# Optimization experiments

Measured on AMD Instinct MI355X. Metric: run time of the kernel, lower is better.

The kernel has to match this reference:

```python
import jax, jax.numpy as jnp
import numpy as np

IN_DIM = 128
OUT_DIM = 128
BATCH = 1024
K = 3        # spline order
INIT_G = 3   # initial number of grid intervals


def setup_inputs() -> dict:
    key = jax.random.key(0)
    k1, k2 = jax.random.split(key)
    x = jax.random.normal(k1, (BATCH, IN_DIM), dtype=jnp.float32)
    # grid as in __init__: arange(-k, G+k+1)*h + (-1), tiled per (in,out) edge
    h = (1.0 - (-1.0)) / INIT_G
    grid_row = jnp.arange(-K, INIT_G + K + 1, dtype=jnp.float32) * h - 1.0  # (G+2k+1,) = (10,)
    grid = jnp.tile(grid_row[None, :], (IN_DIM * OUT_DIM, 1))               # (E, 10)
    n_basis = grid.shape[1] - 1 - K                                          # 6
    c_basis = 0.1 * jax.random.normal(k2, (IN_DIM * OUT_DIM, n_basis), dtype=jnp.float32)
    c_spl = jnp.ones(IN_DIM * OUT_DIM, dtype=jnp.float32)
    c_res = jnp.ones(IN_DIM * OUT_DIM, dtype=jnp.float32)
    return {"x": x, "grid": grid, "c_basis": c_basis, "c_spl": c_spl, "c_res": c_res}


def get_spline_basis(x_ext, grid, k=K):
    # x_ext: (E, B), grid: (E, G)
    g = grid[:, :, None]      # (E, G, 1)
    x = x_ext[:, None, :]     # (E, 1, B)
    b = ((x >= g[:, :-1]) & (x < g[:, 1:])).astype(x_ext.dtype)  # (E, G-1, B)
    for KK in range(1, k + 1):  # Cox-de Boor recursion; k is a small static constant
        left = (x - g[:, :-(KK + 1)]) / (g[:, KK:-1] - g[:, :-(KK + 1)])
        right = (g[:, KK + 1:] - x) / (g[:, KK + 1:] - g[:, 1:-KK])
        b = left * b[:, :-1] + right * b[:, 1:]
    return b  # (E, G-1-k, B)


def reference(x, grid, c_basis, c_spl, c_res):
    batch, in_dim = x.shape
    out_dim = c_spl.shape[0] // in_dim
    # broadcast each input feature to every output: edge index = o*in_dim + i
    x_ext = jnp.broadcast_to(x[:, None, :], (batch, out_dim, in_dim)).reshape(batch, in_dim * out_dim).T  # (E, B)
    res = jax.nn.swish(x_ext).T                                  # (B, E) residual activation
    Bi = get_spline_basis(x_ext, grid, K)                        # (E, 6, B)
    spl = jnp.einsum('ej,ejb->eb', c_basis, Bi).T                # (B, E)
    y = c_spl[None, :] * spl + c_res[None, :] * res              # (B, E)
    y = y.reshape(batch, out_dim, in_dim).sum(axis=2) / in_dim   # (B, out_dim)
    grid_r = grid.reshape(out_dim, in_dim, -1)
    input_norm = grid_r[:, :, -1] - grid_r[:, :, 0] + 1e-05      # (out, in)
    spl_reg = jnp.mean(jnp.abs(spl.reshape(batch, out_dim, in_dim)), axis=0) / input_norm
    return (y, spl_reg)
```

## Files before the change

kernel.cpp:

```cpp
#include <hip/hip_runtime.h>

static constexpr int BATCH   = 1024;
static constexpr int IN_DIM  = 128;
static constexpr int OUT_DIM = 128;
static constexpr int NEDGE   = IN_DIM * OUT_DIM;
static constexpr int Y_SIZE  = BATCH * OUT_DIM;

static constexpr size_t F_OFF  = 0;
static constexpr size_t WY_OFF = (size_t)128 * 1024 * 8;
static constexpr size_t WR_OFF = WY_OFF + (size_t)NEDGE * 8;
static constexpr size_t P_OFF  = WR_OFF + (size_t)NEDGE * 8;
static constexpr size_t C_OFF  = P_OFF + (size_t)NEDGE * 4;
static constexpr size_t P2_OFF = C_OFF + 128;

__global__ __launch_bounds__(256) void k_features(
    const float* __restrict__ x, const float* __restrict__ grid,
    const float* __restrict__ c_basis, const float* __restrict__ c_spl,
    const float* __restrict__ c_res, float* __restrict__ ws)
{
    __shared__ float xs[4][129];
    const int t  = threadIdx.x;
    const int b0 = blockIdx.x * 4;

#pragma unroll
    for (int k = 0; k < 2; ++k) {
        const int f = k * 256 + t;
        xs[f >> 7][f & 127] = x[(size_t)(b0 + (f >> 7)) * IN_DIM + (f & 127)];
    }

    float tg[10];
#pragma unroll
    for (int m = 0; m < 10; ++m) tg[m] = grid[m];

    float inv1[9], inv2[8], inv3[7];
#pragma unroll
    for (int m = 0; m < 9; ++m) inv1[m] = 1.0f / (tg[m + 1] - tg[m]);
#pragma unroll
    for (int m = 0; m < 8; ++m) inv2[m] = 1.0f / (tg[m + 2] - tg[m]);
#pragma unroll
    for (int m = 0; m < 7; ++m) inv3[m] = 1.0f / (tg[m + 3] - tg[m]);

    __syncthreads();

    float4* F4 = reinterpret_cast<float4*>(ws + F_OFF);
    const int brel  = t & 3;
    const int ibase = t >> 2;

#pragma unroll
    for (int k = 0; k < 2; ++k) {
        const int   i  = ibase + k * 64;
        const float xv = xs[brel][i];

        float bb[9];
#pragma unroll
        for (int m = 0; m < 9; ++m)
            bb[m] = (xv >= tg[m] && xv < tg[m + 1]) ? 1.0f : 0.0f;
#pragma unroll
        for (int m = 0; m < 8; ++m)
            bb[m] = (xv - tg[m]) * inv1[m] * bb[m]
                  + (tg[m + 2] - xv) * inv1[m + 1] * bb[m + 1];
#pragma unroll
        for (int m = 0; m < 7; ++m)
            bb[m] = (xv - tg[m]) * inv2[m] * bb[m]
                  + (tg[m + 3] - xv) * inv2[m + 1] * bb[m + 1];
#pragma unroll
        for (int m = 0; m < 6; ++m)
            bb[m] = (xv - tg[m]) * inv3[m] * bb[m]
                  + (tg[m + 4] - xv) * inv3[m + 1] * bb[m + 1];

        const float sw = xv / (1.0f + expf(-xv));
        const size_t g = (size_t)i * 1024 + b0 + brel;
        F4[g * 2 + 0] = make_float4(bb[0], bb[1], bb[2], bb[3]);
        F4[g * 2 + 1] = make_float4(bb[4], bb[5], sw, 0.0f);
    }

    if (t < 64) {
        const int e = blockIdx.x * 64 + t;
        float cb[6];
#pragma unroll
        for (int j = 0; j < 6; ++j) cb[j] = c_basis[(size_t)e * 6 + j];
        const float cs = c_spl[e];
        const float cr = c_res[e];
        const float invfac = 1.0f / ((float)BATCH * (tg[9] - tg[0] + 1e-5f));
        float4* Wy4 = reinterpret_cast<float4*>(ws + WY_OFF);
        float4* Wr4 = reinterpret_cast<float4*>(ws + WR_OFF);
        Wy4[(size_t)e * 2 + 0] = make_float4(cs * cb[0], cs * cb[1], cs * cb[2], cs * cb[3]);
        Wy4[(size_t)e * 2 + 1] = make_float4(cs * cb[4], cs * cb[5], cr, 0.0f);
        Wr4[(size_t)e * 2 + 0] = make_float4(cb[0], cb[1], cb[2], cb[3]);
        Wr4[(size_t)e * 2 + 1] = make_float4(cb[4], cb[5], invfac, 0.0f);
    }
}

__global__ __launch_bounds__(256) void k_main(
    const float* __restrict__ ws_c, float* __restrict__ ws_m)
{
    __shared__ float4 smem4[4096];
    const int t   = threadIdx.x;
    const int blk = blockIdx.x;
    const float4* F4 = reinterpret_cast<const float4*>(ws_c + F_OFF);

    if (blk < 256) {
        const float4* Wy4 = reinterpret_cast<const float4*>(ws_c + WY_OFF);
        const int bt = blk >> 4;
        const int ot = (blk >> 3) & 1;
        const int ic = blk & 7;
        const int b0 = bt * 64, o0 = ot * 64, i0 = ic * 16;
        float4* Fl = smem4;
        float4* Wl = smem4 + 2048;

#pragma unroll
        for (int r = 0; r < 8; ++r) {
            const int idx = r * 256 + t;
            const int ii = idx >> 7, w = idx & 127;
            Fl[ii * 128 + (w ^ ((w >> 3) & 1))] =
                F4[(size_t)(i0 + ii) * 2048 + b0 * 2 + w];
        }
#pragma unroll
        for (int r = 0; r < 8; ++r) {
            const int idx = r * 256 + t;
            const int oo = idx >> 5, w = idx & 31;
            Wl[oo * 32 + (w ^ (((oo >> 2) & 3) << 1))] =
                Wy4[(size_t)(o0 + oo) * 256 + i0 * 2 + w];
        }
        __syncthreads();

        const int bi = t & 15;
        const int og = t >> 4;
        float acc[4][4];
#pragma unroll
        for (int c = 0; c < 4; ++c)
#pragma unroll
            for (int q = 0; q < 4; ++q) acc[c][q] = 0.f;

#pragma unroll 2
        for (int ii = 0; ii < 16; ++ii) {
            float4 fb[4][2], wo[4][2];
#pragma unroll
            for (int c = 0; c < 4; ++c) {
                const int b  = bi + 16 * c;
                const int xr = (b >> 2) & 1;
                fb[c][0] = Fl[ii * 128 + ((b * 2)     ^ xr)];
                fb[c][1] = Fl[ii * 128 + ((b * 2 + 1) ^ xr)];
            }
#pragma unroll
            for (int q = 0; q < 4; ++q) {
                const int o  = og * 4 + q;
                const int xr = (og & 3) << 1;
                wo[q][0] = Wl[o * 32 + ((ii * 2)     ^ xr)];
                wo[q][1] = Wl[o * 32 + ((ii * 2 + 1) ^ xr)];
            }
#pragma unroll
            for (int c = 0; c < 4; ++c)
#pragma unroll
                for (int q = 0; q < 4; ++q) {
                    acc[c][q] += fb[c][0].x * wo[q][0].x + fb[c][0].y * wo[q][0].y
                               + fb[c][0].z * wo[q][0].z + fb[c][0].w * wo[q][0].w
                               + fb[c][1].x * wo[q][1].x + fb[c][1].y * wo[q][1].y
                               + fb[c][1].z * wo[q][1].z + fb[c][1].w * wo[q][1].w;
                }
        }

        float4* P2 = reinterpret_cast<float4*>(ws_m + P2_OFF);
#pragma unroll
        for (int c = 0; c < 4; ++c)
            P2[((size_t)ic * Y_SIZE
                + (size_t)(b0 + bi + 16 * c) * OUT_DIM + o0 + og * 4) >> 2] =
                make_float4(acc[c][0], acc[c][1], acc[c][2], acc[c][3]);
    } else {
        float4* Flds    = smem4;
        float*  partial = reinterpret_cast<float*>(smem4 + 512);
        const int rb = blk - 256;
        const int i  = rb >> 2;
        const int bq = rb & 3;
        const float4* src = F4 + ((size_t)i * 1024 + bq * 256) * 2;
        Flds[t]       = src[t];
        Flds[t + 256] = src[t + 256];

        const int o  = t & 127;
        const int bh = t >> 7;
        const int e  = (o << 7) + i;
        const float4* Wr4 = reinterpret_cast<const float4*>(ws_c + WR_OFF);
        const float4 w0 = Wr4[(size_t)e * 2 + 0];
        const float4 w1 = Wr4[(size_t)e * 2 + 1];
        __syncthreads();

        const float4* fl = &Flds[bh * 256];
        float acc = 0.f;
#pragma unroll 4
        for (int bl = 0; bl < 128; ++bl) {
            const float4 f0 = fl[bl * 2 + 0];
            const float4 f1 = fl[bl * 2 + 1];
            const float spl = f0.x * w0.x + f0.y * w0.y + f0.z * w0.z + f0.w * w0.w
                            + f1.x * w1.x + f1.y * w1.y;
            acc += fabsf(spl);
        }
        partial[t] = acc;
        __syncthreads();
        if (t < 128)
            ws_m[P_OFF + ((size_t)e << 2) + bq] = partial[t] + partial[t + 128];
    }
}

__global__ __launch_bounds__(256) void k_final(
    const float* __restrict__ ws, const float* __restrict__ grid,
    float* __restrict__ out)
{
    const int t   = threadIdx.x;
    const int blk = blockIdx.x;
    if (blk < 128) {
        const int gid = blk * 256 + t;
        const float4* P2 = reinterpret_cast<const float4*>(ws + P2_OFF);
        float4 s = P2[gid];
#pragma unroll
        for (int ic = 1; ic < 8; ++ic) {
            const float4 p = P2[(size_t)ic * (Y_SIZE / 4) + gid];
            s.x += p.x; s.y += p.y; s.z += p.z; s.w += p.w;
        }
        const float sc = 1.0f / (float)IN_DIM;
        reinterpret_cast<float4*>(out)[gid] =
            make_float4(s.x * sc, s.y * sc, s.z * sc, s.w * sc);
    } else {
        const int e = (blk - 128) * 256 + t;
        const float4 p = reinterpret_cast<const float4*>(ws + P_OFF)[e];
        const float invfac = 1.0f / ((float)BATCH * (grid[9] - grid[0] + 1e-5f));
        out[Y_SIZE + e] = (p.x + p.y + p.z + p.w) * invfac;
    }
}

extern "C" void kernel_launch(void* const* d_in, const int* in_sizes, int n_in,
                              void* d_out, int out_size, void* d_ws, size_t ws_size,
                              hipStream_t stream)
{
    const float* x  = (const float*)d_in[0];
    const float* gr = (const float*)d_in[1];
    const float* cb = (const float*)d_in[2];
    const float* cs = (const float*)d_in[3];
    const float* cr = (const float*)d_in[4];
    float* out = (float*)d_out;
    float* ws  = (float*)d_ws;

    k_features<<<256, 256, 0, stream>>>(x, gr, cb, cs, cr, ws);
    k_main<<<768, 256, 0, stream>>>(ws, ws);
    k_final<<<192, 256, 0, stream>>>(ws, gr, out);
}
```

Measured before the change: 84.35 us.

## Fuse feature precompute into main kernel, recomputing spline bases on the fly

Removes the separate feature kernel that wrote a 4 MB basis/swish tensor and the packed weight arrays to workspace. Each main-kernel block now evaluates the B-spline bases and swish directly from x into shared memory, and builds its scaled weights from c_basis, c_spl and c_res. This drops one launch and the global round-trip of the feature tensor. In exchange the basis evaluation is repeated across output tiles, and the weight loads become uncoalesced scalar reads.

```diff
diff --git a/kernel.cpp b/kernel.cpp
--- a/kernel.cpp
+++ b/kernel.cpp
@@ -6,101 +6,51 @@
 static constexpr int NEDGE   = IN_DIM * OUT_DIM;
 static constexpr int Y_SIZE  = BATCH * OUT_DIM;
 
-static constexpr size_t F_OFF  = 0;
-static constexpr size_t WY_OFF = (size_t)128 * 1024 * 8;
-static constexpr size_t WR_OFF = WY_OFF + (size_t)NEDGE * 8;
-static constexpr size_t P_OFF  = WR_OFF + (size_t)NEDGE * 8;
-static constexpr size_t C_OFF  = P_OFF + (size_t)NEDGE * 4;
-static constexpr size_t P2_OFF = C_OFF + 128;
-
-__global__ __launch_bounds__(256) void k_features(
+static constexpr size_t P_OFF  = 0;
+static constexpr size_t P2_OFF = (size_t)NEDGE * 4;
+
+__device__ __forceinline__ void eval_basis(
+    float xv, const float* tg, const float* inv1, const float* inv2,
+    const float* inv3, float* bb )
+{
+#pragma unroll
+    for (int m = 0; m < 9; ++m)
+        bb[m] = (xv >= tg[m] && xv < tg[m + 1]) ? 1.0f : 0.0f;
+#pragma unroll
+    for (int m = 0; m < 8; ++m)
+        bb[m] = (xv - tg[m]) * inv1[m] * bb[m]
+              + (tg[m + 2] - xv) * inv1[m + 1] * bb[m + 1];
+#pragma unroll
+    for (int m = 0; m < 7; ++m)
+        bb[m] = (xv - tg[m]) * inv2[m] * bb[m]
+              + (tg[m + 3] - xv) * inv2[m + 1] * bb[m + 1];
+#pragma unroll
+    for (int m = 0; m < 6; ++m)
+        bb[m] = (xv - tg[m]) * inv3[m] * bb[m]
+              + (tg[m + 4] - xv) * inv3[m + 1] * bb[m + 1];
+}
+
+__global__ __launch_bounds__(256) void k_fused(
     const float* __restrict__ x, const float* __restrict__ grid,
     const float* __restrict__ c_basis, const float* __restrict__ c_spl,
     const float* __restrict__ c_res, float* __restrict__ ws)
 {
-    __shared__ float xs[4][129];
-    const int t  = threadIdx.x;
-    const int b0 = blockIdx.x * 4;
-
-#pragma unroll
-    for (int k = 0; k < 2; ++k) {
-        const int f = k * 256 + t;
-        xs[f >> 7][f & 127] = x[(size_t)(b0 + (f >> 7)) * IN_DIM + (f & 127)];
-    }
-
-    float tg[10];
-#pragma unroll
-    for (int m = 0; m < 10; ++m) tg[m] = grid[m];
-
-    float inv1[9], inv2[8], inv3[7];
-#pragma unroll
-    for (int m = 0; m < 9; ++m) inv1[m] = 1.0f / (tg[m + 1] - tg[m]);
-#pragma unroll
-    for (int m = 0; m < 8; ++m) inv2[m] = 1.0f / (tg[m + 2] - tg[m]);
-#pragma unroll
-    for (int m = 0; m < 7; ++m) inv3[m] = 1.0f / (tg[m + 3] - tg[m]);
-
-    __syncthreads();
-
-    float4* F4 = reinterpret_cast<float4*>(ws + F_OFF);
-    const int brel  = t & 3;
-    const int ibase = t >> 2;
-
-#pragma unroll
-    for (int k = 0; k < 2; ++k) {
-        const int   i  = ibase + k * 64;
-        const float xv = xs[brel][i];
-
-        float bb[9];
-#pragma unroll
-        for (int m = 0; m < 9; ++m)
-            bb[m] = (xv >= tg[m] && xv < tg[m + 1]) ? 1.0f : 0.0f;
-#pragma unroll
-        for (int m = 0; m < 8; ++m)
-            bb[m] = (xv - tg[m]) * inv1[m] * bb[m]
-                  + (tg[m + 2] - xv) * inv1[m + 1] * bb[m + 1];
-#pragma unroll
-        for (int m = 0; m < 7; ++m)
-            bb[m] = (xv - tg[m]) * inv2[m] * bb[m]
-                  + (tg[m + 3] - xv) * inv2[m + 1] * bb[m + 1];
-#pragma unroll
-        for (int m = 0; m < 6; ++m)
-            bb[m] = (xv - tg[m]) * inv3[m] * bb[m]
-                  + (tg[m + 4] - xv) * inv3[m + 1] * bb[m + 1];
-
-        const float sw = xv / (1.0f + expf(-xv));
-        const size_t g = (size_t)i * 1024 + b0 + brel;
-        F4[g * 2 + 0] = make_float4(bb[0], bb[1], bb[2], bb[3]);
-        F4[g * 2 + 1] = make_float4(bb[4], bb[5], sw, 0.0f);
-    }
-
-    if (t < 64) {
-        const int e = blockIdx.x * 64 + t;
-        float cb[6];
-#pragma unroll
-        for (int j = 0; j < 6; ++j) cb[j] = c_basis[(size_t)e * 6 + j];
-        const float cs = c_spl[e];
-        const float cr = c_res[e];
-        const float invfac = 1.0f / ((float)BATCH * (tg[9] - tg[0] + 1e-5f));
-        float4* Wy4 = reinterpret_cast<float4*>(ws + WY_OFF);
-        float4* Wr4 = reinterpret_cast<float4*>(ws + WR_OFF);
-        Wy4[(size_t)e * 2 + 0] = make_float4(cs * cb[0], cs * cb[1], cs * cb[2], cs * cb[3]);
-        Wy4[(size_t)e * 2 + 1] = make_float4(cs * cb[4], cs * cb[5], cr, 0.0f);
-        Wr4[(size_t)e * 2 + 0] = make_float4(cb[0], cb[1], cb[2], cb[3]);
-        Wr4[(size_t)e * 2 + 1] = make_float4(cb[4], cb[5], invfac, 0.0f);
-    }
-}
-
-__global__ __launch_bounds__(256) void k_main(
-    const float* __restrict__ ws_c, float* __restrict__ ws_m)
-{
     __shared__ float4 smem4[4096];
     const int t   = threadIdx.x;
     const int blk = blockIdx.x;
-    const float4* F4 = reinterpret_cast<const float4*>(ws_c + F_OFF);
+
+    float tg[10];
+#pragma unroll
+    for (int m = 0; m < 10; ++m) tg[m] = grid[m];
+    float inv1[9], inv2[8], inv3[7];
+#pragma unroll
+    for (int m = 0; m < 9; ++m) inv1[m] = 1.0f / (tg[m + 1] - tg[m]);
+#pragma unroll
+    for (int m = 0; m < 8; ++m) inv2[m] = 1.0f / (tg[m + 2] - tg[m]);
+#pragma unroll
+    for (int m = 0; m < 7; ++m) inv3[m] = 1.0f / (tg[m + 3] - tg[m]);
 
     if (blk < 256) {
-        const float4* Wy4 = reinterpret_cast<const float4*>(ws_c + WY_OFF);
         const int bt = blk >> 4;
         const int ot = (blk >> 3) & 1;
         const int ic = blk & 7;
@@ -108,19 +58,30 @@
         float4* Fl = smem4;
         float4* Wl = smem4 + 2048;
 
-#pragma unroll
-        for (int r = 0; r < 8; ++r) {
-            const int idx = r * 256 + t;
-            const int ii = idx >> 7, w = idx & 127;
-            Fl[ii * 128 + (w ^ ((w >> 3) & 1))] =
-                F4[(size_t)(i0 + ii) * 2048 + b0 * 2 + w];
-        }
-#pragma unroll
-        for (int r = 0; r < 8; ++r) {
-            const int idx = r * 256 + t;
-            const int oo = idx >> 5, w = idx & 31;
-            Wl[oo * 32 + (w ^ (((oo >> 2) & 3) << 1))] =
-                Wy4[(size_t)(o0 + oo) * 256 + i0 * 2 + w];
+        const int bl  = t & 63;
+        const int iig = t >> 6;
+        const int oo  = t >> 2;
+#pragma unroll
+        for (int k = 0; k < 4; ++k) {
+            const int   ii = iig + 4 * k;
+            const float xv = x[(size_t)(b0 + bl) * IN_DIM + i0 + ii];
+            float bb[9];
+            eval_basis(xv, tg, inv1, inv2, inv3, bb);
+            const float sw = xv / (1.0f + expf(-xv));
+            const int xr = (bl >> 2) & 1;
+            Fl[ii * 128 + ((bl * 2)     ^ xr)] = make_float4(bb[0], bb[1], bb[2], bb[3]);
+            Fl[ii * 128 + ((bl * 2 + 1) ^ xr)] = make_float4(bb[4], bb[5], sw, 0.f);
+
+            const int iw = (t & 3) + 4 * k;
+            const int e  = (o0 + oo) * IN_DIM + i0 + iw;
+            const float cs = c_spl[e];
+            const float cr = c_res[e];
+            const float* cb = c_basis + (size_t)e * 6;
+            const int xw = ((oo >> 2) & 3) << 1;
+            Wl[oo * 32 + ((iw * 2)     ^ xw)] =
+                make_float4(cs * cb[0], cs * cb[1], cs * cb[2], cs * cb[3]);
+            Wl[oo * 32 + ((iw * 2 + 1) ^ xw)] =
+                make_float4(cs * cb[4], cs * cb[5], cr, 0.f);
         }
         __syncthreads();
 
@@ -160,7 +121,7 @@
                 }
         }
 
-        float4* P2 = reinterpret_cast<float4*>(ws_m + P2_OFF);
+        float4* P2 = reinterpret_cast<float4*>(ws + P2_OFF);
 #pragma unroll
         for (int c = 0; c < 4; ++c)
             P2[((size_t)ic * Y_SIZE
@@ -172,16 +133,19 @@
         const int rb = blk - 256;
         const int i  = rb >> 2;
         const int bq = rb & 3;
-        const float4* src = F4 + ((size_t)i * 1024 + bq * 256) * 2;
-        Flds[t]       = src[t];
-        Flds[t + 256] = src[t + 256];
+
+        const float xv = x[(size_t)(bq * 256 + t) * IN_DIM + i];
+        float bb[9];
+        eval_basis(xv, tg, inv1, inv2, inv3, bb);
+        Flds[t * 2]     = make_float4(bb[0], bb[1], bb[2], bb[3]);
+        Flds[t * 2 + 1] = make_float4(bb[4], bb[5], 0.f, 0.f);
 
         const int o  = t & 127;
         const int bh = t >> 7;
         const int e  = (o << 7) + i;
-        const float4* Wr4 = reinterpret_cast<const float4*>(ws_c + WR_OFF);
-        const float4 w0 = Wr4[(size_t)e * 2 + 0];
-        const float4 w1 = Wr4[(size_t)e * 2 + 1];
+        const float* cb = c_basis + (size_t)e * 6;
+        const float4 w0 = make_float4(cb[0], cb[1], cb[2], cb[3]);
+        const float w1x = cb[4], w1y = cb[5];
         __syncthreads();
 
         const float4* fl = &Flds[bh * 256];
@@ -191,13 +155,14 @@
             const float4 f0 = fl[bl * 2 + 0];
             const float4 f1 = fl[bl * 2 + 1];
             const float spl = f0.x * w0.x + f0.y * w0.y + f0.z * w0.z + f0.w * w0.w
-                            + f1.x * w1.x + f1.y * w1.y;
+                            + f1.x * w1x + f1.y * w1y;
             acc += fabsf(spl);
         }
         partial[t] = acc;
         __syncthreads();
         if (t < 128)
-            ws_m[P_OFF + ((size_t)e << 2) + bq] = partial[t] + partial[t + 128];
+            ws[P_OFF + ((size_t)((t & 127) << 7) + i) * 4 + bq] =
+                partial[t] + partial[t + 128];
     }
 }
 
@@ -239,7 +204,6 @@
     float* out = (float*)d_out;
     float* ws  = (float*)d_ws;
 
-    k_features<<<256, 256, 0, stream>>>(x, gr, cb, cs, cr, ws);
-    k_main<<<768, 256, 0, stream>>>(ws, ws);
+    k_fused<<<768, 256, 0, stream>>>(x, gr, cb, cs, cr, ws);
     k_final<<<192, 256, 0, stream>>>(ws, gr, out);
 }
```

Result: faster. 80.90 us (-4.1%).
